# Kernel tuning notes

Hardware: AMD Instinct MI355X
Metric: run time of the kernel (lower is better)

## Reference

```python
import jax, jax.numpy as jnp
import numpy as np
from jax import lax

SEQ, BSZ, INP, HID = 512, 64, 512, 512


def _lstm_scan(xs, h0, c0, Wih, Whh, bih, bhh, reverse):
    """Run an LSTMCell recurrence over time. xs: (T, B, I). Returns (ys:(T,B,H), hT, cT)."""
    def step(carry, x):
        h, c = carry
        gates = x @ Wih.T + bih + h @ Whh.T + bhh  # (B, 4H)
        i, f, g, o = jnp.split(gates, 4, axis=-1)
        c_new = jax.nn.sigmoid(f) * c + jax.nn.sigmoid(i) * jnp.tanh(g)
        h_new = jax.nn.sigmoid(o) * jnp.tanh(c_new)
        return (h_new, c_new), h_new
    (hT, cT), ys = lax.scan(step, (h0, c0), xs, reverse=reverse)
    return ys, hT, cT


def setup_inputs() -> dict:
    key = jax.random.key(0)
    ks = jax.random.split(key, 13)
    s = 0.05  # keep weights small so gates stay in a sane range
    return {
        "input_": jax.random.normal(ks[0], (SEQ, BSZ, INP), jnp.float32),
        "h0_f": jax.random.normal(ks[1], (BSZ, HID), jnp.float32),
        "c0_f": jax.random.normal(ks[2], (BSZ, HID), jnp.float32),
        "h0_b": jax.random.normal(ks[3], (BSZ, HID), jnp.float32),
        "c0_b": jax.random.normal(ks[4], (BSZ, HID), jnp.float32),
        "W_ih_f": jax.random.normal(ks[5], (4 * HID, INP), jnp.float32) * s,
        "W_hh_f": jax.random.normal(ks[6], (4 * HID, HID), jnp.float32) * s,
        "b_ih_f": jax.random.normal(ks[7], (4 * HID,), jnp.float32) * s,
        "b_hh_f": jax.random.normal(ks[8], (4 * HID,), jnp.float32) * s,
        "W_ih_b": jax.random.normal(ks[9], (4 * HID, INP), jnp.float32) * s,
        "W_hh_b": jax.random.normal(ks[10], (4 * HID, HID), jnp.float32) * s,
        "b_ih_b": jax.random.normal(ks[11], (4 * HID,), jnp.float32) * s,
        "b_hh_b": jax.random.normal(ks[12], (4 * HID,), jnp.float32) * s,
    }


def reference(input_, h0_f, c0_f, h0_b, c0_b,
              W_ih_f, W_hh_f, b_ih_f, b_hh_f,
              W_ih_b, W_hh_b, b_ih_b, b_hh_b):
    # forward direction
    ys_f, hT_f, cT_f = _lstm_scan(input_, h0_f, c0_f, W_ih_f, W_hh_f, b_ih_f, b_hh_f, reverse=False)
    # reverse direction (scan from last step; outputs stored at original positions)
    ys_b, hT_b, cT_b = _lstm_scan(input_, h0_b, c0_b, W_ih_b, W_hh_b, b_ih_b, b_hh_b, reverse=True)
    out = jnp.concatenate([ys_f, ys_b], axis=-1)  # (T, B, 2H)
    return out, hT_f, cT_f, hT_b, cT_b
```

## Files before the change

### kernel.cpp

```cpp
#include <hip/hip_runtime.h>
#include <cstdint>
#include <cstddef>

#define T_ 512
#define B_ 64
#define I_ 512
#define H_ 512
#define SENT32 0x7FC07FC0

typedef __attribute__((ext_vector_type(8))) short short8;
typedef __attribute__((ext_vector_type(4))) float f32x4;
typedef __attribute__((ext_vector_type(4))) int i32x4;

#define MFMA(a, b, c) __builtin_amdgcn_mfma_f32_16x16x32_bf16((a), (b), (c), 0, 0, 0)

__device__ __forceinline__ unsigned short f2bf(float f) {
  union { float f; unsigned u; } v; v.f = f;
  unsigned r = v.u + 0x7fffu + ((v.u >> 16) & 1u);
  return (unsigned short)(r >> 16);
}

__device__ __forceinline__ float sigm(float x) { return 1.0f / (1.0f + __expf(-x)); }
__device__ __forceinline__ float tanh_fast(float x) {
  float e = __expf(2.0f * x);
  return 1.0f - 2.0f / (e + 1.0f);
}

__device__ __forceinline__ short8 loadWfrag(const float* __restrict__ p) {
  float4 a = ((const float4*)p)[0];
  float4 b = ((const float4*)p)[1];
  short8 r;
  r[0] = (short)f2bf(a.x); r[1] = (short)f2bf(a.y);
  r[2] = (short)f2bf(a.z); r[3] = (short)f2bf(a.w);
  r[4] = (short)f2bf(b.x); r[5] = (short)f2bf(b.y);
  r[6] = (short)f2bf(b.z); r[7] = (short)f2bf(b.w);
  return r;
}

__device__ __forceinline__ void st16(void* p, i32x4 v) {
  asm volatile("global_store_dwordx4 %0, %1, off sc0 sc1" :: "v"(p), "v"(v) : "memory");
}

#define LDH1(i, OFF)                                                          \
  asm volatile("global_load_dwordx4 %0, %1, off offset:" OFF " sc0 sc1"       \
               : "=v"(hf[i]) : "v"(hsrc) : "memory")
#define LDH_ALL()                                                             \
  LDH1(0, "0"); LDH1(1, "64"); LDH1(2, "128"); LDH1(3, "192");                \
  LDH1(4, "256"); LDH1(5, "320"); LDH1(6, "384"); LDH1(7, "448");             \
  LDH1(8, "512"); LDH1(9, "576"); LDH1(10, "640"); LDH1(11, "704");           \
  LDH1(12, "768"); LDH1(13, "832"); LDH1(14, "896"); LDH1(15, "960")
#define LDH_IF(i, OFF) if (!((done >> i) & 1u)) { LDH1(i, OFF); }
#define LDH_MISSING()                                                         \
  LDH_IF(0, "0") LDH_IF(1, "64") LDH_IF(2, "128") LDH_IF(3, "192")            \
  LDH_IF(4, "256") LDH_IF(5, "320") LDH_IF(6, "384") LDH_IF(7, "448")         \
  LDH_IF(8, "512") LDH_IF(9, "576") LDH_IF(10, "640") LDH_IF(11, "704")       \
  LDH_IF(12, "768") LDH_IF(13, "832") LDH_IF(14, "896") LDH_IF(15, "960")

#define LDX1(i, OFF)                                                          \
  asm volatile("global_load_dwordx4 %0, %1, off offset:" OFF                  \
               : "=v"(xf[i]) : "v"(xsrc) : "memory")
#define LDX_ALL()                                                             \
  LDX1(0, "0"); LDX1(1, "64"); LDX1(2, "128"); LDX1(3, "192");                \
  LDX1(4, "256"); LDX1(5, "320"); LDX1(6, "384"); LDX1(7, "448");             \
  LDX1(8, "512"); LDX1(9, "576"); LDX1(10, "640"); LDX1(11, "704");           \
  LDX1(12, "768"); LDX1(13, "832"); LDX1(14, "896"); LDX1(15, "960")

__global__ void prep_x(const float4* __restrict__ x, ushort4* __restrict__ xb) {
  int i = blockIdx.x * 256 + threadIdx.x;
  float4 v = x[i];
  ushort4 o;
  o.x = f2bf(v.x); o.y = f2bf(v.y); o.z = f2bf(v.z); o.w = f2bf(v.w);
  xb[i] = o;
}

__global__ void prep_init(const float* __restrict__ h0f, const float* __restrict__ h0b,
                          unsigned short* __restrict__ hbufs) {
  int i = blockIdx.x * 256 + threadIdx.x;
  int dir = i >> 18;
  int rem = i & 262143;
  int buf = rem >> 15;
  int idx = rem & 32767;
  const float* src = dir ? h0b : h0f;
  hbufs[i] = (buf == 0) ? f2bf(src[idx]) : (unsigned short)0x7FC0;
}

__global__ __launch_bounds__(256, 1) void lstm_coop(
    const unsigned short* __restrict__ xbf,
    unsigned short* __restrict__ hbufs,
    const float* __restrict__ Wih_f, const float* __restrict__ Whh_f,
    const float* __restrict__ bih_f, const float* __restrict__ bhh_f,
    const float* __restrict__ c0_f,
    const float* __restrict__ Wih_b, const float* __restrict__ Whh_b,
    const float* __restrict__ bih_b, const float* __restrict__ bhh_b,
    const float* __restrict__ c0_b,
    float* __restrict__ out) {
  const int tid = threadIdx.x;
  const int wave = tid >> 6;
  const int lane = tid & 63;
  const int quad = lane >> 4;
  const int lm = lane & 15;

  const int wg = blockIdx.x;
  const int dir = wg >> 6;
  const int jw = wg & 63;
  const int hb = jw * 8;

  const float* Wih = dir ? Wih_b : Wih_f;
  const float* Whh = dir ? Whh_b : Whh_f;
  const float* bih = dir ? bih_b : bih_f;
  const float* bhh = dir ? bhh_b : bhh_f;
  const float* c0  = dir ? c0_b  : c0_f;

  short8 wx[2][16], wh[2][16];
#pragma unroll
  for (int nt = 0; nt < 2; ++nt) {
    int nl = nt * 16 + lm;
    int row = (nl >> 3) * 512 + hb + (nl & 7);
#pragma unroll
    for (int kk = 0; kk < 16; ++kk) {
      int k = kk * 32 + quad * 8;
      wx[nt][kk] = loadWfrag(Wih + (size_t)row * 512 + k);
      wh[nt][kk] = loadWfrag(Whh + (size_t)row * 512 + k);
    }
  }

  const int u = lm & 7;
  float bsum[4];
#pragma unroll
  for (int g = 0; g < 4; ++g)
    bsum[g] = bih[g * 512 + hb + u] + bhh[g * 512 + hb + u];

  const int b0 = wave * 16 + quad * 4;
  float creg[4], hlast[4];
#pragma unroll
  for (int r = 0; r < 4; ++r) {
    creg[r] = c0[(size_t)(b0 + r) * 512 + hb + u];
    hlast[r] = 0.f;
  }

  char* hdir = (char*)hbufs + (size_t)dir * 8 * 65536;
  const int arow = wave * 16 + lm;
  const char* hload_lane = hdir + (size_t)arow * 1024 + quad * 16;
  const int r0 = (lm & 2) | ((lm & 4) >> 2);
  char* hstore_lane = hdir + (size_t)(wave * 16 + quad * 4 + r0) * 1024 + jw * 16;
  const bool wr = (lm < 8) && ((lm & 1) == 0);
  const char* xb_lane = (const char*)xbf + (size_t)arow * 1024 + quad * 16;

  const i32x4 sent4 = {SENT32, SENT32, SENT32, SENT32};

  short8 xf[16];
  {
    const char* xsrc = xb_lane + (size_t)(dir ? 511 : 0) * 65536;
    LDX_ALL();
  }
  asm volatile("s_waitcnt vmcnt(0)" ::: "memory");

  for (int s = 0; s < 512; ++s) {
    const int t = dir ? (511 - s) : s;

    if (wr) st16(hstore_lane + (size_t)((s + 2) & 7) * 65536, sent4);

    asm volatile("s_waitcnt vmcnt(3)" ::: "memory");
    __builtin_amdgcn_sched_barrier(0);

    const char* hsrc = hload_lane + (size_t)(s & 7) * 65536;
    short8 hf[16];
    LDH_ALL();
    __builtin_amdgcn_sched_barrier(0);

    f32x4 acc0 = {0.f, 0.f, 0.f, 0.f};
    f32x4 acc1 = {0.f, 0.f, 0.f, 0.f};
#pragma unroll
    for (int kk = 0; kk < 16; ++kk) {
      acc0 = MFMA(xf[kk], wx[0][kk], acc0);
      acc1 = MFMA(xf[kk], wx[1][kk], acc1);
    }

    {
      unsigned done = 0;
      while (true) {
        asm volatile("s_waitcnt vmcnt(0)" ::: "memory");
        __builtin_amdgcn_sched_barrier(0);
        unsigned newly = 0;
#pragma unroll
        for (int kk = 0; kk < 16; ++kk) {
          if (!((done >> kk) & 1u)) {
            i32x4 w = __builtin_bit_cast(i32x4, hf[kk]);
            int ok = (w[0] != SENT32) & (w[1] != SENT32) &
                     (w[2] != SENT32) & (w[3] != SENT32);
            if (__all(ok)) newly |= 1u << kk;
          }
        }
        done |= newly;
        if (done != 0xFFFFu) { LDH_MISSING(); }
#pragma unroll
        for (int kk = 0; kk < 16; ++kk) {
          if ((newly >> kk) & 1u) {
            acc0 = MFMA(hf[kk], wh[0][kk], acc0);
            acc1 = MFMA(hf[kk], wh[1][kk], acc1);
          }
        }
        if (done == 0xFFFFu) break;
      }
    }

    float hv[4];
#pragma unroll
    for (int r = 0; r < 4; ++r) {
      float p0 = __shfl_xor(acc0[r], 8, 64);
      float p1 = __shfl_xor(acc1[r], 8, 64);
      float gi  = (lm < 8 ? acc0[r] : p0) + bsum[0];
      float gfr = (lm < 8 ? p0 : acc0[r]) + bsum[1];
      float gg  = (lm < 8 ? acc1[r] : p1) + bsum[2];
      float go  = (lm < 8 ? p1 : acc1[r]) + bsum[3];
      float cn = sigm(gfr) * creg[r] + sigm(gi) * tanh_fast(gg);
      creg[r] = cn;
      hv[r] = sigm(go) * tanh_fast(cn);
      hlast[r] = hv[r];
    }
    float q0 = __shfl_xor(hv[0], 1, 64), q1 = __shfl_xor(hv[1], 1, 64);
    float q2 = __shfl_xor(hv[2], 1, 64), q3 = __shfl_xor(hv[3], 1, 64);

    {
      const int ue = ((lm & 1) == 0);
      int V0 = ue ? ((int)f2bf(hv[0]) | ((int)f2bf(q0) << 16))
                  : ((int)f2bf(q0) | ((int)f2bf(hv[0]) << 16));
      int V1 = ue ? ((int)f2bf(hv[1]) | ((int)f2bf(q1) << 16))
                  : ((int)f2bf(q1) | ((int)f2bf(hv[1]) << 16));
      int V2 = ue ? ((int)f2bf(hv[2]) | ((int)f2bf(q2) << 16))
                  : ((int)f2bf(q2) | ((int)f2bf(hv[2]) << 16));
      int V3 = ue ? ((int)f2bf(hv[3]) | ((int)f2bf(q3) << 16))
                  : ((int)f2bf(q3) | ((int)f2bf(hv[3]) << 16));
      int P0 = __shfl_xor(V0, 2, 64), P1 = __shfl_xor(V1, 2, 64);
      int P2 = __shfl_xor(V2, 2, 64), P3 = __shfl_xor(V3, 2, 64);
      int X0 = ((lm & 2) == 0) ? V0 : P2;
      int X1 = ((lm & 2) == 0) ? P0 : V2;
      int X2 = ((lm & 2) == 0) ? V1 : P3;
      int X3 = ((lm & 2) == 0) ? P1 : V3;
      int Y0 = __shfl_xor(X0, 4, 64), Y1 = __shfl_xor(X1, 4, 64);
      int Y2 = __shfl_xor(X2, 4, 64), Y3 = __shfl_xor(X3, 4, 64);
      i32x4 Z;
      if ((lm & 4) == 0) { Z[0] = X0; Z[1] = X1; Z[2] = Y0; Z[3] = Y1; }
      else               { Z[0] = Y2; Z[1] = Y3; Z[2] = X2; Z[3] = X3; }
      if (wr) st16(hstore_lane + (size_t)((s + 1) & 7) * 65536, Z);
    }

    {
      int sn = s + 1 < 512 ? s + 1 : 511;
      int tn = dir ? (511 - sn) : sn;
      const char* xsrc = xb_lane + (size_t)tn * 65536;
      LDX_ALL();
    }

    if (lm < 8) {
      const int sel = lm & 1;
      float2 vA = sel ? make_float2(q2, hv[2]) : make_float2(hv[0], q0);
      float2 vB = sel ? make_float2(q3, hv[3]) : make_float2(hv[1], q1);
      float* ob = out + (size_t)t * 65536 + dir * 512 + hb + (lm & ~1);
      *(float2*)(ob + (size_t)(b0 + 2 * sel) * 1024) = vA;
      *(float2*)(ob + (size_t)(b0 + 2 * sel + 1) * 1024) = vB;
    }
  }

  if (lm < 8) {
    float* obase = out + 33554432 + dir * 65536;
#pragma unroll
    for (int r = 0; r < 4; ++r) {
      obase[(size_t)(b0 + r) * 512 + hb + u] = hlast[r];
      obase[32768 + (size_t)(b0 + r) * 512 + hb + u] = creg[r];
    }
  }
}

extern "C" void kernel_launch(void* const* d_in, const int* in_sizes, int n_in,
                              void* d_out, int out_size, void* d_ws, size_t ws_size,
                              hipStream_t stream) {
  (void)in_sizes; (void)n_in; (void)out_size; (void)ws_size;

  const float* X     = (const float*)d_in[0];
  const float* h0_f  = (const float*)d_in[1];
  const float* c0_f  = (const float*)d_in[2];
  const float* h0_b  = (const float*)d_in[3];
  const float* c0_b  = (const float*)d_in[4];
  const float* Wih_f = (const float*)d_in[5];
  const float* Whh_f = (const float*)d_in[6];
  const float* bih_f = (const float*)d_in[7];
  const float* bhh_f = (const float*)d_in[8];
  const float* Wih_b = (const float*)d_in[9];
  const float* Whh_b = (const float*)d_in[10];
  const float* bih_b = (const float*)d_in[11];
  const float* bhh_b = (const float*)d_in[12];
  float* out = (float*)d_out;

  unsigned short* xbf   = (unsigned short*)d_ws;
  unsigned short* hbufs = (unsigned short*)((char*)d_ws + 33554432);

  prep_x<<<16384, 256, 0, stream>>>((const float4*)X, (ushort4*)xbf);
  prep_init<<<2048, 256, 0, stream>>>(h0_f, h0_b, hbufs);

  lstm_coop<<<dim3(128), dim3(256), 0, stream>>>(
      xbf, hbufs,
      Wih_f, Whh_f, bih_f, bhh_f, c0_f,
      Wih_b, Whh_b, bih_b, bhh_b, c0_b,
      out);
}
```

Measured before the change: 3.157 ms.

## Probe missing h chunks with dword loads before refetching full vectors

The spin-wait on hidden-state chunks published by other waves changes strategy. When many chunks are still missing, it reissues only cheap 4-byte probe loads and refetches the full 16-byte chunk only after its probe sees no sentinel; with six or fewer missing it refetches directly. The next-step x prefetch moves after the output stores, and the wait before the h loads is relaxed to vmcnt(17). The aim is to cut memory traffic and latency in the cross-wave polling loop, at the cost of an extra round trip for probed chunks and more complex wait-count bookkeeping.

```diff
diff --git a/kernel.cpp b/kernel.cpp
--- a/kernel.cpp
+++ b/kernel.cpp
@@ -49,12 +49,32 @@
   LDH1(4, "256"); LDH1(5, "320"); LDH1(6, "384"); LDH1(7, "448");             \
   LDH1(8, "512"); LDH1(9, "576"); LDH1(10, "640"); LDH1(11, "704");           \
   LDH1(12, "768"); LDH1(13, "832"); LDH1(14, "896"); LDH1(15, "960")
-#define LDH_IF(i, OFF) if (!((done >> i) & 1u)) { LDH1(i, OFF); }
-#define LDH_MISSING()                                                         \
-  LDH_IF(0, "0") LDH_IF(1, "64") LDH_IF(2, "128") LDH_IF(3, "192")            \
-  LDH_IF(4, "256") LDH_IF(5, "320") LDH_IF(6, "384") LDH_IF(7, "448")         \
-  LDH_IF(8, "512") LDH_IF(9, "576") LDH_IF(10, "640") LDH_IF(11, "704")       \
-  LDH_IF(12, "768") LDH_IF(13, "832") LDH_IF(14, "896") LDH_IF(15, "960")
+#define LDH_IFM(i, OFF, M) if (((M) >> i) & 1u) { LDH1(i, OFF); }
+#define LDH_MASK(M)                                                           \
+  LDH_IFM(0, "0", M) LDH_IFM(1, "64", M) LDH_IFM(2, "128", M)                 \
+  LDH_IFM(3, "192", M) LDH_IFM(4, "256", M) LDH_IFM(5, "320", M)              \
+  LDH_IFM(6, "384", M) LDH_IFM(7, "448", M) LDH_IFM(8, "512", M)              \
+  LDH_IFM(9, "576", M) LDH_IFM(10, "640", M) LDH_IFM(11, "704", M)            \
+  LDH_IFM(12, "768", M) LDH_IFM(13, "832", M) LDH_IFM(14, "896", M)           \
+  LDH_IFM(15, "960", M)
+#define PRB1(i, OFF)                                                          \
+  asm volatile("global_load_dword %0, %1, off offset:" OFF " sc0 sc1"         \
+               : "=v"(pr[i]) : "v"(hsrc) : "memory")
+#define PRB_IFM(i, OFF, M) if (((M) >> i) & 1u) { PRB1(i, OFF); }
+#define PRB_MASK(M)                                                           \
+  PRB_IFM(0, "0", M) PRB_IFM(1, "64", M) PRB_IFM(2, "128", M)                 \
+  PRB_IFM(3, "192", M) PRB_IFM(4, "256", M) PRB_IFM(5, "320", M)              \
+  PRB_IFM(6, "384", M) PRB_IFM(7, "448", M) PRB_IFM(8, "512", M)              \
+  PRB_IFM(9, "576", M) PRB_IFM(10, "640", M) PRB_IFM(11, "704", M)            \
+  PRB_IFM(12, "768", M) PRB_IFM(13, "832", M) PRB_IFM(14, "896", M)           \
+  PRB_IFM(15, "960", M)
+#define CONSUME(M)                                                            \
+  _Pragma("unroll")                                                           \
+  for (int kk = 0; kk < 16; ++kk)                                             \
+    if (((M) >> kk) & 1u) {                                                   \
+      acc0 = MFMA(hf[kk], wh[0][kk], acc0);                                   \
+      acc1 = MFMA(hf[kk], wh[1][kk], acc1);                                   \
+    }
 
 #define LDX1(i, OFF)                                                          \
   asm volatile("global_load_dwordx4 %0, %1, off offset:" OFF                  \
@@ -160,12 +180,11 @@
 
     if (wr) st16(hstore_lane + (size_t)((s + 2) & 7) * 65536, sent4);
 
-    asm volatile("s_waitcnt vmcnt(3)" ::: "memory");
-    __builtin_amdgcn_sched_barrier(0);
-
     const char* hsrc = hload_lane + (size_t)(s & 7) * 65536;
     short8 hf[16];
     LDH_ALL();
+
+    asm volatile("s_waitcnt vmcnt(17)" ::: "memory");
     __builtin_amdgcn_sched_barrier(0);
 
     f32x4 acc0 = {0.f, 0.f, 0.f, 0.f};
@@ -177,30 +196,37 @@
     }
 
     {
-      unsigned done = 0;
+      unsigned done = 0, infl = 0xFFFFu;
+      int pr[16];
       while (true) {
         asm volatile("s_waitcnt vmcnt(0)" ::: "memory");
         __builtin_amdgcn_sched_barrier(0);
         unsigned newly = 0;
 #pragma unroll
-        for (int kk = 0; kk < 16; ++kk) {
-          if (!((done >> kk) & 1u)) {
+        for (int kk = 0; kk < 16; ++kk)
+          if ((infl >> kk) & 1u) {
             i32x4 w = __builtin_bit_cast(i32x4, hf[kk]);
             int ok = (w[0] != SENT32) & (w[1] != SENT32) &
                      (w[2] != SENT32) & (w[3] != SENT32);
             if (__all(ok)) newly |= 1u << kk;
           }
-        }
         done |= newly;
-        if (done != 0xFFFFu) { LDH_MISSING(); }
-#pragma unroll
-        for (int kk = 0; kk < 16; ++kk) {
-          if ((newly >> kk) & 1u) {
-            acc0 = MFMA(hf[kk], wh[0][kk], acc0);
-            acc1 = MFMA(hf[kk], wh[1][kk], acc1);
+        if (done == 0xFFFFu) { CONSUME(newly); break; }
+        unsigned miss = 0xFFFFu & ~done;
+        unsigned probed = miss & ~infl;
+        unsigned readym = 0;
+#pragma unroll
+        for (int kk = 0; kk < 16; ++kk)
+          if ((probed >> kk) & 1u) {
+            if (__all(pr[kk] != SENT32)) readym |= 1u << kk;
           }
-        }
-        if (done == 0xFFFFu) break;
+        unsigned refull, reprobe;
+        if (__builtin_popcount(miss) <= 6) { refull = miss; reprobe = 0; }
+        else { refull = readym; reprobe = miss & ~readym; }
+        LDH_MASK(refull);
+        PRB_MASK(reprobe);
+        infl = refull;
+        CONSUME(newly);
       }
     }
 
@@ -245,13 +271,6 @@
       if (wr) st16(hstore_lane + (size_t)((s + 1) & 7) * 65536, Z);
     }
 
-    {
-      int sn = s + 1 < 512 ? s + 1 : 511;
-      int tn = dir ? (511 - sn) : sn;
-      const char* xsrc = xb_lane + (size_t)tn * 65536;
-      LDX_ALL();
-    }
-
     if (lm < 8) {
       const int sel = lm & 1;
       float2 vA = sel ? make_float2(q2, hv[2]) : make_float2(hv[0], q0);
@@ -259,6 +278,13 @@
       float* ob = out + (size_t)t * 65536 + dir * 512 + hb + (lm & ~1);
       *(float2*)(ob + (size_t)(b0 + 2 * sel) * 1024) = vA;
       *(float2*)(ob + (size_t)(b0 + 2 * sel + 1) * 1024) = vB;
+    }
+
+    {
+      int sn = s + 1 < 512 ? s + 1 : 511;
+      int tn = dir ? (511 - sn) : sn;
+      const char* xsrc = xb_lane + (size_t)tn * 65536;
+      LDX_ALL();
     }
   }
 
```

Measured after the change: 7.041 ms. 2.23x slower.
